# Kernel tuning notes

Hardware: AMD Instinct MI355X
Metric: run time of the kernel (lower is better)

## Reference

```python
import jax, jax.numpy as jnp
import numpy as np

EPS = 1e-5


def spline_conv(x, src, dst, pseudo, W, root, bias, num_nodes, K=5):
    """Degree-1 open B-spline conv (torch_spline_conv semantics), mean aggregation.
    W: [kernel_total, Cin, Cout]. kernel_total==1 means trivial basis (kernel_size=1)."""
    E = src.shape[0]
    Cin = x.shape[1]
    KT = W.shape[0]
    x_j = x[src]                                            # [E, Cin] edge gather
    deg = jax.ops.segment_sum(jnp.ones((E,), x.dtype), dst, num_segments=num_nodes)
    deg = jnp.maximum(deg, 1.0)
    if KT == 1:
        agg = jax.ops.segment_sum(x_j, dst, num_segments=num_nodes)
        out = (agg / deg[:, None]) @ W[0]
    else:
        v = pseudo * (K - 1)                                # open spline: v in [0, K-1]
        f = jnp.clip(jnp.floor(v), 0.0, K - 2)
        frac = v - f                                        # [E, 2]
        fi = f.astype(jnp.int32)
        # bucket basis-weighted source features by (kernel_index, dst) then one dense einsum
        h = jnp.zeros((KT * num_nodes, Cin), x.dtype)
        for s0 in (0, 1):
            for s1 in (0, 1):
                b0 = frac[:, 0] if s0 else 1.0 - frac[:, 0]
                b1 = frac[:, 1] if s1 else 1.0 - frac[:, 1]
                basis = b0 * b1                             # [E]
                wi = (fi[:, 0] + s0) + K * (fi[:, 1] + s1)  # [E] kernel index in [0,25)
                seg = wi * num_nodes + dst
                h = h + jax.ops.segment_sum(basis[:, None] * x_j, seg,
                                            num_segments=KT * num_nodes)
        agg = jnp.einsum('knc,kco->no', h.reshape(KT, num_nodes, Cin), W)
        out = agg / deg[:, None]
    return out + x @ root + bias


def batch_norm(x, gamma, beta):
    m = x.mean(axis=0)
    var = jnp.mean((x - m) ** 2, axis=0)
    return gamma * (x - m) * jax.lax.rsqrt(var + EPS) + beta


def setup_inputs() -> dict:
    key = jax.random.key(0)
    ks = jax.random.split(key, 8)
    N, E, Cin, Cout = 50000, 800000, 32, 64
    x = jax.random.normal(ks[0], (N, Cin), jnp.float32)
    edge_index = jax.random.randint(ks[1], (2, E), 0, N, jnp.int32)
    edge_attr = jax.random.uniform(ks[2], (E, 2), jnp.float32)
    s = 0.1
    return {
        'x': x, 'edge_index': edge_index, 'edge_attr': edge_attr,
        'w1': jax.random.normal(ks[3], (25, Cin, Cout), jnp.float32) * s,
        'r1': jax.random.normal(ks[4], (Cin, Cout), jnp.float32) * s,
        'b1': jnp.zeros((Cout,), jnp.float32),
        'g1': jnp.ones((Cout,), jnp.float32),
        'beta1': jnp.zeros((Cout,), jnp.float32),
        'w2': jax.random.normal(ks[5], (25, Cout, Cout), jnp.float32) * s,
        'r2': jax.random.normal(ks[6], (Cout, Cout), jnp.float32) * s,
        'b2': jnp.zeros((Cout,), jnp.float32),
        'g2': jnp.ones((Cout,), jnp.float32),
        'beta2': jnp.zeros((Cout,), jnp.float32),
        'ws': jax.random.normal(ks[7], (1, Cin, Cout), jnp.float32) * s,
        'rs': jax.random.normal(jax.random.fold_in(key, 99), (Cin, Cout), jnp.float32) * s,
        'bs': jnp.zeros((Cout,), jnp.float32),
        'gs': jnp.ones((Cout,), jnp.float32),
        'betas': jnp.zeros((Cout,), jnp.float32),
    }


def reference(x, edge_index, edge_attr, w1, r1, b1, g1, beta1,
              w2, r2, b2, g2, beta2, ws, rs, bs, gs, betas):
    N = x.shape[0]
    src, dst = edge_index[0], edge_index[1]
    h = jax.nn.elu(batch_norm(spline_conv(x, src, dst, edge_attr, w1, r1, b1, N), g1, beta1))
    left = batch_norm(spline_conv(h, src, dst, edge_attr, w2, r2, b2, N), g2, beta2)
    short = batch_norm(spline_conv(x, src, dst, edge_attr, ws, rs, bs, N), gs, betas)
    return jax.nn.elu(left + short)
```

## Files before the change

### kernel.cpp

```cpp
#include <hip/hip_runtime.h>

#define NN 50000
#define NE 800000
#define DBINS 1024

typedef __attribute__((ext_vector_type(8))) short bf16x8;
typedef __attribute__((ext_vector_type(4))) float f32x4;
typedef __attribute__((ext_vector_type(2))) float f32x2;

__device__ __forceinline__ unsigned short f2bf(float f) {
    union { float f; unsigned u; } v; v.f = f;
    unsigned r = v.u + 0x7FFFu + ((v.u >> 16) & 1u);
    return (unsigned short)(r >> 16);
}

__device__ __forceinline__ int4 ld_ep2(const int4* ep, unsigned idx, int which) {
    return *(const int4*)((const char*)ep + (size_t)(idx * 32u + (unsigned)which * 16u));
}
__device__ __forceinline__ unsigned ld_xu(const unsigned* X, unsigned byteoff) {
    return *(const unsigned*)((const char*)X + (size_t)byteoff);
}

__device__ __forceinline__ f32x2 unpack2(unsigned u) {
    union { unsigned u; float f; } a, b;
    a.u = u << 16;
    b.u = u & 0xFFFF0000u;
    return f32x2{a.f, b.f};
}

__device__ __forceinline__ f32x2 pk_mul_hib(f32x2 w, f32x2 x) {
    f32x2 d;
    asm("v_pk_mul_f32 %0, %1, %2 op_sel:[1,0] op_sel_hi:[1,1]"
        : "=v"(d) : "v"(w), "v"(x));
    return d;
}
__device__ __forceinline__ void pk_fma_lob(f32x2& h, f32x2 w, f32x2 t) {
    asm("v_pk_fma_f32 %0, %1, %2, %0 op_sel:[0,0,0] op_sel_hi:[0,1,1]"
        : "+v"(h) : "v"(w), "v"(t));
}

__device__ __forceinline__ int us_idx(int kk, int r, int m) {
    return kk*544 + (r >> 3)*136 + m*8 + (r & 7);
}
__device__ __forceinline__ int us8_idx(int kk, int r, int m) {
    return kk*272 + (r >> 3)*68 + m*8 + (r & 7);
}

template<bool HS>
__device__ __forceinline__ void edge_acc2(f32x2* h, f32x2& hs,
                                          const int4& pa, const int4& pb, f32x2 x) {
    f32x2 wxy[5];
    wxy[0] = unpack2((unsigned)pa.y);
    wxy[1] = unpack2((unsigned)pa.z);
    wxy[2] = unpack2((unsigned)pa.w);
    wxy[3] = unpack2((unsigned)pb.x);
    wxy[4] = unpack2((unsigned)pb.y);
    if (HS) hs += x;
#pragma unroll
    for (int r1 = 0; r1 < 5; ++r1) {
        f32x2 ty = pk_mul_hib(wxy[r1], x);
#pragma unroll
        for (int r0 = 0; r0 < 5; ++r0)
            pk_fma_lob(h[r1*5 + r0], wxy[r0], ty);
    }
}

__device__ __forceinline__ float eh_reduce(f32x2 v, int eh, int stride) {
    float mine  = eh ? v.y : v.x;
    float other = eh ? v.x : v.y;
    return mine + __shfl_xor(other, stride);
}

__global__ __launch_bounds__(256) void k_zero(int* degi, int* cur, float* stats,
                                              int* dcnt, int* dcur,
                                              unsigned* xz, unsigned* hz) {
    int i = blockIdx.x*256 + threadIdx.x;
    int stride = gridDim.x*256;
    for (int j = i; j < NN; j += stride) { degi[j] = 0; cur[j] = 0; }
    if (i < 384) stats[i] = 0.f;
    if (i < DBINS) { dcnt[i] = 0; dcur[i] = 0; }
    if (i < 16) xz[i] = 0u;
    if (i < 32) hz[i] = 0u;
}

__global__ __launch_bounds__(256) void k_hist(const int* __restrict__ dst, int* degi) {
    int e = blockIdx.x*256 + threadIdx.x;
    if (e < NE) atomicAdd(&degi[dst[e]], 1);
}

__global__ __launch_bounds__(256) void k_scan_block(const int* __restrict__ degi,
                                                    int* off, int* bsum) {
    __shared__ int sh[256];
    int t = threadIdx.x;
    int base = blockIdx.x * 1024;
    int v[4]; int s = 0;
#pragma unroll
    for (int j = 0; j < 4; j++) {
        int idx = base + t*4 + j;
        v[j] = (idx < NN) ? ((degi[idx] + 3) & ~3) : 0;
        s += v[j];
    }
    sh[t] = s; __syncthreads();
    for (int ofs = 1; ofs < 256; ofs <<= 1) {
        int x = (t >= ofs) ? sh[t - ofs] : 0;
        __syncthreads();
        sh[t] += x;
        __syncthreads();
    }
    int ex = sh[t] - s;
#pragma unroll
    for (int j = 0; j < 4; j++) {
        int idx = base + t*4 + j;
        if (idx < NN) off[idx] = ex;
        ex += v[j];
    }
    if (t == 255) bsum[blockIdx.x] = sh[255];
}

__global__ __launch_bounds__(256) void k_dhist(const int* __restrict__ degi, int* dcnt) {
    __shared__ int lh[DBINS];
    int t = threadIdx.x;
#pragma unroll
    for (int j = 0; j < DBINS/256; ++j) lh[t + 256*j] = 0;
    __syncthreads();
    int n = blockIdx.x*256 + t;
    if (n < NN) atomicAdd(&lh[min(degi[n], DBINS-1)], 1);
    __syncthreads();
#pragma unroll
    for (int j = 0; j < DBINS/256; ++j) {
        int b = t + 256*j;
        if (lh[b]) atomicAdd(&dcnt[b], lh[b]);
    }
}

__global__ __launch_bounds__(256) void k_topscan(const int* __restrict__ bsum,
                                                 int* bpre, int nb,
                                                 const int* __restrict__ dcnt,
                                                 int* dbase) {
    __shared__ int sh[256];
    int t = threadIdx.x;
    if (blockIdx.x == 0) {
        int s = (t < nb) ? bsum[t] : 0;
        sh[t] = s; __syncthreads();
        for (int ofs = 1; ofs < 256; ofs <<= 1) {
            int x = (t >= ofs) ? sh[t - ofs] : 0;
            __syncthreads();
            sh[t] += x;
            __syncthreads();
        }
        if (t < nb) bpre[t] = sh[t] - s;
    } else {
        int v[4]; int s = 0;
#pragma unroll
        for (int j = 0; j < 4; j++) { v[j] = dcnt[t*4 + j]; s += v[j]; }
        sh[t] = s; __syncthreads();
        for (int ofs = 1; ofs < 256; ofs <<= 1) {
            int x = (t >= ofs) ? sh[t - ofs] : 0;
            __syncthreads();
            sh[t] += x;
            __syncthreads();
        }
        int ex = sh[t] - s;
#pragma unroll
        for (int j = 0; j < 4; j++) { dbase[t*4 + j] = ex; ex += v[j]; }
    }
}

__global__ __launch_bounds__(256) void k_scan_add(int* off, const int* __restrict__ bpre,
                                                  const int* __restrict__ degi) {
    int i = blockIdx.x*256 + threadIdx.x;
    if (i < NN) {
        int v = off[i] + bpre[i >> 10];
        off[i] = v;
        if (i == NN - 1) off[NN] = v + ((degi[i] + 3) & ~3);
    }
}

__global__ __launch_bounds__(256) void k_pscatter_pad(const int* __restrict__ degi,
                                                      const int* __restrict__ dbase,
                                                      int* dcur, int* perm,
                                                      const int* __restrict__ off,
                                                      int4* __restrict__ ep) {
    __shared__ int lh[DBINS];
    __shared__ int lb[DBINS];
    int t = threadIdx.x;
#pragma unroll
    for (int j = 0; j < DBINS/256; ++j) lh[t + 256*j] = 0;
    __syncthreads();
    int n = blockIdx.x*256 + t;
    int d = 0, lr = 0;
    bool act = (n < NN);
    if (act) {
        d = min(degi[n], DBINS-1);
        lr = atomicAdd(&lh[d], 1);
    }
    __syncthreads();
#pragma unroll
    for (int j = 0; j < DBINS/256; ++j) {
        int b = t + 256*j;
        int c = lh[b];
        lb[b] = c ? atomicAdd(&dcur[b], c) : 0;
    }
    __syncthreads();
    if (act) {
        perm[dbase[d] + lb[d] + lr] = n;
        int base = off[n] + degi[n];
        int end  = off[n + 1];
        for (int p = base; p < end; ++p) {
            ep[2*p]     = make_int4(NN, 0, 0, 0);
            ep[2*p + 1] = make_int4(0, 0, 0, 0);
        }
    }
}

__global__ __launch_bounds__(256) void k_scatter(const int* __restrict__ src,
                                                 const int* __restrict__ dst,
                                                 const float* __restrict__ ea,
                                                 const int* __restrict__ off, int* cur,
                                                 int4* __restrict__ ep) {
    int e = blockIdx.x*256 + threadIdx.x;
    if (e >= NE) return;
    int d = dst[e];
    int p = off[d] + atomicAdd(&cur[d], 1);
    float v0 = ea[2*e]     * 4.f;
    float v1 = ea[2*e + 1] * 4.f;
    unsigned w[5];
#pragma unroll
    for (int r = 0; r < 5; ++r) {
        float wx = fmaxf(1.f - fabsf(v0 - (float)r), 0.f);
        float wy = fmaxf(1.f - fabsf(v1 - (float)r), 0.f);
        w[r] = (unsigned)f2bf(wx) | ((unsigned)f2bf(wy) << 16);
    }
    ep[2*p]     = make_int4(src[e], (int)w[0], (int)w[1], (int)w[2]);
    ep[2*p + 1] = make_int4((int)w[3], (int)w[4], 0, 0);
}

__device__ __forceinline__ void wprep_body(int tid, const float* W, const float* root,
                                           int KTC, unsigned short* Wb) {
    int lane = tid & 63, cot = (tid >> 6) & 3, kk = tid >> 8;
    int co = 16*cot + (lane & 15);
    int kbase = kk*32 + ((lane >> 4) * 8);
    union { unsigned short s[8]; uint4 v; } u;
#pragma unroll
    for (int j = 0; j < 8; j++) {
        int k = kbase + j;
        float val = (k < KTC) ? W[(size_t)k*64 + co] : root[(size_t)(k - KTC)*64 + co];
        u.s[j] = f2bf(val);
    }
    *(uint4*)(Wb + (size_t)tid * 8) = u.v;
}

__global__ __launch_bounds__(256) void k_prep(const float* __restrict__ x,
                                              unsigned short* __restrict__ xb,
                                              const float* __restrict__ w1,
                                              const float* __restrict__ r1,
                                              unsigned short* Wb1,
                                              const float* __restrict__ wsN,
                                              const float* __restrict__ rs,
                                              unsigned short* WbS,
                                              const float* __restrict__ w2,
                                              const float* __restrict__ r2,
                                              unsigned short* Wb2) {
    int b = blockIdx.x, t = threadIdx.x;
    if (b < 1563) {
        int i = b*256 + t;
        if (i >= NN*8) return;
        float4 v = ((const float4*)x)[i];
        uint2 pk;
        pk.x = (unsigned)f2bf(v.x) | ((unsigned)f2bf(v.y) << 16);
        pk.y = (unsigned)f2bf(v.z) | ((unsigned)f2bf(v.w) << 16);
        ((uint2*)xb)[i] = pk;
    } else if (b < 1589) {
        wprep_body((b - 1563)*256 + t, w1, r1, 800, Wb1);
    } else if (b < 1591) {
        wprep_body((b - 1589)*256 + t, wsN, rs, 32, WbS);
    } else {
        wprep_body((b - 1591)*256 + t, w2, r2, 1600, Wb2);
    }
}

__global__ __launch_bounds__(512, 4) void k_conv1s(
        const unsigned* __restrict__ Xbf,
        const int* __restrict__ off,
        const int* __restrict__ degi,
        const int4* __restrict__ ep,
        const int* __restrict__ perm,
        const unsigned short* __restrict__ Wb1,
        const unsigned short* __restrict__ WbS,
        const float* __restrict__ b1,
        const float* __restrict__ bs,
        float* __restrict__ agg1,
        float* __restrict__ aggS) {
    __shared__ __align__(16) unsigned short hb[28*544];
    const int t = threadIdx.x;
    const int g = t >> 5;
    const int q = t & 31;
    const int chp = q & 15;
    const int eh = q >> 4;
    const int n0 = blockIdx.x * 16;
    const int n = perm[n0 + g];

    f32x2 h[25], hs = {0.f, 0.f};
#pragma unroll
    for (int i = 0; i < 25; ++i) h[i] = f32x2{0.f, 0.f};

    const int ebeg = off[n], eend = off[n + 1];
    const float rdeg = 1.f / (float)max(degi[n], 1);

    for (int i = ebeg; i < eend; i += 4) {
        const unsigned i0 = (unsigned)(i + eh), i1 = (unsigned)(i + 2 + eh);
        int4 a0 = ld_ep2(ep, i0, 0), b0 = ld_ep2(ep, i0, 1);
        int4 a1 = ld_ep2(ep, i1, 0), b1 = ld_ep2(ep, i1, 1);
        unsigned u0 = ld_xu(Xbf, (unsigned)a0.x * 64u + (unsigned)chp * 4u);
        unsigned u1 = ld_xu(Xbf, (unsigned)a1.x * 64u + (unsigned)chp * 4u);
        edge_acc2<true>(h, hs, a0, b0, unpack2(u0));
        edge_acc2<true>(h, hs, a1, b1, unpack2(u1));
    }

    const int c = 2*chp + eh;
    const int bw = us_idx(0, c, g);
#pragma unroll
    for (int wi = 0; wi < 25; ++wi)
        hb[wi*544 + bw] = f2bf(eh_reduce(h[wi], eh, 16) * rdeg);
    hb[26*544 + bw] = f2bf(eh_reduce(hs, eh, 16) * rdeg);
    {
        unsigned ux = Xbf[(unsigned)n * 16u + (unsigned)chp];
        unsigned short xb = eh ? (unsigned short)(ux >> 16)
                               : (unsigned short)(ux & 0xFFFFu);
        hb[25*544 + bw] = xb;
        hb[27*544 + bw] = xb;
    }
    __syncthreads();

    const int lane = t & 63, w = t >> 6;
    const int m = lane & 15, qq = lane >> 4;
    const int co = (w & 3)*16 + m;
    const int4 pn = ((const int4*)perm)[(n0 >> 2) + qq];
    const int prow[4] = {pn.x, pn.y, pn.z, pn.w};
    if (w < 4) {
        f32x4 acc = {0.f, 0.f, 0.f, 0.f};
        for (int kk = 0; kk < 26; ++kk) {
            bf16x8 av = *(const bf16x8*)&hb[kk*544 + qq*136 + m*8];
            bf16x8 bv = *(const bf16x8*)(Wb1 + (size_t)((kk*4 + w)*64 + lane) * 8);
            acc = __builtin_amdgcn_mfma_f32_16x16x32_bf16(av, bv, acc, 0, 0, 0);
        }
        const float bb = b1[co];
#pragma unroll
        for (int r = 0; r < 4; ++r)
            agg1[(size_t)prow[r]*64 + co] = acc[r] + bb;
    } else {
        f32x4 accs = {0.f, 0.f, 0.f, 0.f};
#pragma unroll
        for (int s = 0; s < 2; ++s) {
            bf16x8 av = *(const bf16x8*)&hb[(26 + s)*544 + qq*136 + m*8];
            bf16x8 bv = *(const bf16x8*)(WbS + (size_t)((s*4 + (w & 3))*64 + lane) * 8);
            accs = __builtin_amdgcn_mfma_f32_16x16x32_bf16(av, bv, accs, 0, 0, 0);
        }
        const float bb = bs[co];
#pragma unroll
        for (int r = 0; r < 4; ++r)
            aggS[(size_t)prow[r]*64 + co] = accs[r] + bb;
    }
}

__global__ __launch_bounds__(256, 5) void k_conv2(
        const unsigned* __restrict__ Xbf,
        const int* __restrict__ off,
        const int* __restrict__ degi,
        const int4* __restrict__ ep,
        const int* __restrict__ perm,
        const unsigned short* __restrict__ Wb2,
        const float* __restrict__ b2,
        float* __restrict__ agg) {
    __shared__ __align__(16) unsigned short hb[52*272 + 256];
    const int t = threadIdx.x, lane = t & 63, w = t >> 6;
    const int n0 = blockIdx.x * 8;
    const int chp = lane & 31, eh = lane >> 5;
    const int c = 2*chp + eh;
    const int kh = c >> 5, r = c & 31;

#pragma unroll
    for (int nn = 0; nn < 2; ++nn) {
        const int g = 2*w + nn;
        const int n = perm[n0 + g];
        f32x2 h[25]; f32x2 hsd = {0.f, 0.f};
#pragma unroll
        for (int i = 0; i < 25; ++i) h[i] = f32x2{0.f, 0.f};

        const int ebeg = off[n], eend = off[n + 1];
        const float rdeg = 1.f / (float)max(degi[n], 1);

        for (int i = ebeg; i < eend; i += 4) {
            const unsigned i0 = (unsigned)(i + eh), i1 = (unsigned)(i + 2 + eh);
            int4 a0 = ld_ep2(ep, i0, 0), b0 = ld_ep2(ep, i0, 1);
            int4 a1 = ld_ep2(ep, i1, 0), b1 = ld_ep2(ep, i1, 1);
            unsigned u0 = ld_xu(Xbf, (unsigned)a0.x * 128u + (unsigned)chp * 4u);
            unsigned u1 = ld_xu(Xbf, (unsigned)a1.x * 128u + (unsigned)chp * 4u);
            edge_acc2<false>(h, hsd, a0, b0, unpack2(u0));
            edge_acc2<false>(h, hsd, a1, b1, unpack2(u1));
        }

        const int bw = us8_idx(0, r, g);
#pragma unroll
        for (int wi = 0; wi < 25; ++wi)
            hb[(wi*2 + kh)*272 + bw] = f2bf(eh_reduce(h[wi], eh, 32) * rdeg);
        {
            unsigned ux = Xbf[(unsigned)n * 32u + (unsigned)chp];
            hb[(50 + kh)*272 + bw] =
                (unsigned short)(eh ? (ux >> 16) : (ux & 0xFFFFu));
        }
    }
    __syncthreads();

    const int m = lane & 15, qq = lane >> 4;
    f32x4 acc = {0.f, 0.f, 0.f, 0.f};
    for (int kk = 0; kk < 52; ++kk) {
        bf16x8 av = *(const bf16x8*)&hb[kk*272 + qq*68 + m*8];
        bf16x8 bv = *(const bf16x8*)(Wb2 + (size_t)((kk*4 + w)*64 + lane) * 8);
        acc = __builtin_amdgcn_mfma_f32_16x16x32_bf16(av, bv, acc, 0, 0, 0);
    }
    if (qq < 2) {
        const int4 pn = ((const int4*)perm)[(n0 >> 2) + qq];
        const int prow[4] = {pn.x, pn.y, pn.z, pn.w};
        const int co = w*16 + m;
        const float bb = b2[co];
#pragma unroll
        for (int rr = 0; rr < 4; ++rr)
            agg[(size_t)prow[rr]*64 + co] = acc[rr] + bb;
    }
}

__global__ __launch_bounds__(256) void k_bnstats(const float* __restrict__ agg, float* stats) {
    __shared__ float sh0[256], sh1[256];
    int t = threadIdx.x;
    float s = 0.f, ss = 0.f;
    int stride = gridDim.x * 256;
    for (int i = blockIdx.x*256 + t; i < NN*64; i += stride) {
        float v = agg[i];
        s += v; ss += v*v;
    }
    sh0[t] = s; sh1[t] = ss;
    __syncthreads();
    if (t < 64) {
        float a = sh0[t] + sh0[t+64] + sh0[t+128] + sh0[t+192];
        float b = sh1[t] + sh1[t+64] + sh1[t+128] + sh1[t+192];
        atomicAdd(&stats[t], a);
        atomicAdd(&stats[64 + t], b);
    }
}

__global__ __launch_bounds__(256) void k_bnstats2(const float* __restrict__ a1,
                                                  const float* __restrict__ as,
                                                  float* stats) {
    __shared__ float sh0[256], sh1[256];
    int t = threadIdx.x;
    const float* src = (blockIdx.x < 256) ? a1 : as;
    float* dst = (blockIdx.x < 256) ? (stats + 128) : (stats + 256);
    int bid = (blockIdx.x < 256) ? blockIdx.x : blockIdx.x - 256;
    float s = 0.f, ss = 0.f;
    for (int i = bid*256 + t; i < NN*64; i += 256*256) {
        float v = src[i];
        s += v; ss += v*v;
    }
    sh0[t] = s; sh1[t] = ss;
    __syncthreads();
    if (t < 64) {
        float a = sh0[t] + sh0[t+64] + sh0[t+128] + sh0[t+192];
        float b = sh1[t] + sh1[t+64] + sh1[t+128] + sh1[t+192];
        atomicAdd(&dst[t], a);
        atomicAdd(&dst[64 + t], b);
    }
}

__device__ __forceinline__ float eluf(float u) { return u > 0.f ? u : expm1f(u); }

__global__ __launch_bounds__(256) void k_bn_elu(const float* __restrict__ agg,
                                                const float* __restrict__ stats,
                                                const float* __restrict__ gamma,
                                                const float* __restrict__ beta,
                                                unsigned short* __restrict__ outb) {
    int i = blockIdx.x*256 + threadIdx.x;
    if (i >= NN*16) return;
    float4 v = ((const float4*)agg)[i];
    float r[4] = {v.x, v.y, v.z, v.w};
    int c0 = (i << 2) & 63;
#pragma unroll
    for (int j = 0; j < 4; j++) {
        int c = c0 + j;
        float mu = stats[c] * (1.f/NN);
        float var = stats[64 + c] * (1.f/NN) - mu*mu;
        float sc = gamma[c] * rsqrtf(fmaxf(var, 0.f) + 1e-5f);
        r[j] = eluf((r[j] - mu)*sc + beta[c]);
    }
    uint2 pk;
    pk.x = (unsigned)f2bf(r[0]) | ((unsigned)f2bf(r[1]) << 16);
    pk.y = (unsigned)f2bf(r[2]) | ((unsigned)f2bf(r[3]) << 16);
    ((uint2*)outb)[i] = pk;
}

__global__ __launch_bounds__(256) void k_bn_final(const float* __restrict__ a2,
                                                  const float* __restrict__ st2,
                                                  const float* __restrict__ g2,
                                                  const float* __restrict__ be2,
                                                  const float* __restrict__ as,
                                                  const float* __restrict__ sts,
                                                  const float* __restrict__ gs,
                                                  const float* __restrict__ bes,
                                                  float* __restrict__ out) {
    int i = blockIdx.x*256 + threadIdx.x;
    if (i >= NN*16) return;
    float4 v2 = ((const float4*)a2)[i];
    float4 vs = ((const float4*)as)[i];
    float r2v[4] = {v2.x, v2.y, v2.z, v2.w};
    float rsv[4] = {vs.x, vs.y, vs.z, vs.w};
    float o[4];
    int c0 = (i << 2) & 63;
#pragma unroll
    for (int j = 0; j < 4; j++) {
        int c = c0 + j;
        float mu2 = st2[c] * (1.f/NN);
        float var2 = st2[64 + c] * (1.f/NN) - mu2*mu2;
        float sc2 = g2[c] * rsqrtf(fmaxf(var2, 0.f) + 1e-5f);
        float mus = sts[c] * (1.f/NN);
        float vars = sts[64 + c] * (1.f/NN) - mus*mus;
        float scs = gs[c] * rsqrtf(fmaxf(vars, 0.f) + 1e-5f);
        float u = (r2v[j] - mu2)*sc2 + be2[c] + (rsv[j] - mus)*scs + bes[c];
        o[j] = eluf(u);
    }
    ((float4*)out)[i] = make_float4(o[0], o[1], o[2], o[3]);
}

extern "C" void kernel_launch(void* const* d_in, const int* in_sizes, int n_in,
                              void* d_out, int out_size, void* d_ws, size_t ws_size,
                              hipStream_t stream) {
    const float* x   = (const float*)d_in[0];
    const int*   ei  = (const int*)d_in[1];
    const float* ea  = (const float*)d_in[2];
    const float* w1  = (const float*)d_in[3];
    const float* r1  = (const float*)d_in[4];
    const float* b1  = (const float*)d_in[5];
    const float* g1  = (const float*)d_in[6];
    const float* be1 = (const float*)d_in[7];
    const float* w2  = (const float*)d_in[8];
    const float* r2  = (const float*)d_in[9];
    const float* b2  = (const float*)d_in[10];
    const float* g2  = (const float*)d_in[11];
    const float* be2 = (const float*)d_in[12];
    const float* wsN = (const float*)d_in[13];
    const float* rs  = (const float*)d_in[14];
    const float* bs  = (const float*)d_in[15];
    const float* gs  = (const float*)d_in[16];
    const float* bes = (const float*)d_in[17];
    const int* srcp = ei;
    const int* dstp = ei + NE;

    char* wsb = (char*)d_ws;
    size_t o = 0;
    auto alloc = [&](size_t bytes) -> char* {
        char* p = wsb + o;
        o += (bytes + 255) & ~(size_t)255;
        return p;
    };
    int*    degi    = (int*)   alloc((size_t)NN * 4);
    int*    cur     = (int*)   alloc((size_t)NN * 4);
    int*    off     = (int*)   alloc((size_t)(NN + 1) * 4);
    int*    bsum    = (int*)   alloc(256 * 4);
    int*    bpre    = (int*)   alloc(256 * 4);
    int*    dcnt    = (int*)   alloc(DBINS * 4);
    int*    dcur    = (int*)   alloc(DBINS * 4);
    int*    dbase   = (int*)   alloc(DBINS * 4);
    int*    perm    = (int*)   alloc((size_t)NN * 4);
    int4*   ep      = (int4*)  alloc(((size_t)NE + 3*NN + 64) * 32);
    unsigned short* Wb1 = (unsigned short*)alloc(26 * 4096);
    unsigned short* WbS = (unsigned short*)alloc(2 * 4096);
    unsigned short* Wb2 = (unsigned short*)alloc(52 * 4096);
    float*  agg1    = (float*) alloc((size_t)NN * 64 * 4);
    float*  aggS    = (float*) alloc((size_t)NN * 64 * 4);
    unsigned short* h1bf = (unsigned short*)alloc((size_t)(NN + 1) * 64 * 2);
    unsigned short* xbf  = (unsigned short*)alloc((size_t)(NN + 1) * 32 * 2);
    float*  stats   = (float*) alloc(384 * 4);
    (void)ws_size; (void)in_sizes; (void)n_in; (void)out_size;

    float* out = (float*)d_out;

    k_zero<<<196, 256, 0, stream>>>(degi, cur, stats, dcnt, dcur,
                                    (unsigned*)(xbf + (size_t)NN * 32),
                                    (unsigned*)(h1bf + (size_t)NN * 64));
    k_hist<<<3125, 256, 0, stream>>>(dstp, degi);
    k_scan_block<<<49, 256, 0, stream>>>(degi, off, bsum);
    k_dhist<<<196, 256, 0, stream>>>(degi, dcnt);
    k_topscan<<<2, 256, 0, stream>>>(bsum, bpre, 49, dcnt, dbase);
    k_scan_add<<<196, 256, 0, stream>>>(off, bpre, degi);
    k_pscatter_pad<<<196, 256, 0, stream>>>(degi, dbase, dcur, perm, off, ep);
    k_scatter<<<3125, 256, 0, stream>>>(srcp, dstp, ea, off, cur, ep);

    k_prep<<<1643, 256, 0, stream>>>(x, xbf, w1, r1, Wb1, wsN, rs, WbS, w2, r2, Wb2);

    k_conv1s<<<3125, 512, 0, stream>>>((const unsigned*)xbf, off, degi, ep, perm,
                                       Wb1, WbS, b1, bs, agg1, aggS);
    k_bnstats<<<256, 256, 0, stream>>>(agg1, stats);
    k_bn_elu<<<3125, 256, 0, stream>>>(agg1, stats, g1, be1, h1bf);

    k_conv2<<<6250, 256, 0, stream>>>((const unsigned*)h1bf, off, degi, ep, perm,
                                      Wb2, b2, agg1);
    k_bnstats2<<<512, 256, 0, stream>>>(agg1, aggS, stats);
    k_bn_final<<<3125, 256, 0, stream>>>(agg1, stats + 128, g2, be2,
                                         aggS, stats + 256, gs, bes, out);
}
```

Measured before the change: 427.6 us.

## Restructure conv2 to one 32-lane group per node, 16 nodes per block

k_conv2 now runs 512-thread blocks covering 16 nodes, with each 32-thread half-wave processing one node's edges sequentially over all 64 channels. Before, each wave handled 2 nodes with edges split across half-waves and a cross-lane reduction. This removes the eh_reduce shuffle and gives the MFMA tiles a full 16 rows instead of 8 useful ones. The staged hidden buffer is written in two halves with extra barriers so shared memory stays small, but only 4 of the 8 waves issue MFMAs, and per-node serial edge loops may worsen imbalance across degrees.

```diff
diff --git a/kernel.cpp b/kernel.cpp
--- a/kernel.cpp
+++ b/kernel.cpp
@@ -41,9 +41,6 @@
 
 __device__ __forceinline__ int us_idx(int kk, int r, int m) {
     return kk*544 + (r >> 3)*136 + m*8 + (r & 7);
-}
-__device__ __forceinline__ int us8_idx(int kk, int r, int m) {
-    return kk*272 + (r >> 3)*68 + m*8 + (r & 7);
 }
 
 template<bool HS>
@@ -363,7 +360,7 @@
     }
 }
 
-__global__ __launch_bounds__(256, 5) void k_conv2(
+__global__ __launch_bounds__(512, 6) void k_conv2(
         const unsigned* __restrict__ Xbf,
         const int* __restrict__ off,
         const int* __restrict__ degi,
@@ -372,62 +369,75 @@
         const unsigned short* __restrict__ Wb2,
         const float* __restrict__ b2,
         float* __restrict__ agg) {
-    __shared__ __align__(16) unsigned short hb[52*272 + 256];
+    __shared__ __align__(16) unsigned short hb[26*544];
+    unsigned* hb32 = (unsigned*)hb;
     const int t = threadIdx.x, lane = t & 63, w = t >> 6;
-    const int n0 = blockIdx.x * 8;
-    const int chp = lane & 31, eh = lane >> 5;
-    const int c = 2*chp + eh;
-    const int kh = c >> 5, r = c & 31;
-
-#pragma unroll
-    for (int nn = 0; nn < 2; ++nn) {
-        const int g = 2*w + nn;
-        const int n = perm[n0 + g];
-        f32x2 h[25]; f32x2 hsd = {0.f, 0.f};
-#pragma unroll
-        for (int i = 0; i < 25; ++i) h[i] = f32x2{0.f, 0.f};
-
-        const int ebeg = off[n], eend = off[n + 1];
-        const float rdeg = 1.f / (float)max(degi[n], 1);
-
-        for (int i = ebeg; i < eend; i += 4) {
-            const unsigned i0 = (unsigned)(i + eh), i1 = (unsigned)(i + 2 + eh);
-            int4 a0 = ld_ep2(ep, i0, 0), b0 = ld_ep2(ep, i0, 1);
-            int4 a1 = ld_ep2(ep, i1, 0), b1 = ld_ep2(ep, i1, 1);
-            unsigned u0 = ld_xu(Xbf, (unsigned)a0.x * 128u + (unsigned)chp * 4u);
-            unsigned u1 = ld_xu(Xbf, (unsigned)a1.x * 128u + (unsigned)chp * 4u);
-            edge_acc2<false>(h, hsd, a0, b0, unpack2(u0));
-            edge_acc2<false>(h, hsd, a1, b1, unpack2(u1));
-        }
-
-        const int bw = us8_idx(0, r, g);
-#pragma unroll
-        for (int wi = 0; wi < 25; ++wi)
-            hb[(wi*2 + kh)*272 + bw] = f2bf(eh_reduce(h[wi], eh, 32) * rdeg);
-        {
-            unsigned ux = Xbf[(unsigned)n * 32u + (unsigned)chp];
-            hb[(50 + kh)*272 + bw] =
-                (unsigned short)(eh ? (ux >> 16) : (ux & 0xFFFFu));
-        }
+    const int n0 = blockIdx.x * 16;
+    const int g = t >> 5;
+    const int chp = t & 31;
+    const int n = perm[n0 + g];
+
+    f32x2 h[25];
+#pragma unroll
+    for (int i = 0; i < 25; ++i) h[i] = f32x2{0.f, 0.f};
+
+    const int ebeg = off[n], eend = off[n + 1];
+    const float rdeg = 1.f / (float)max(degi[n], 1);
+
+    for (int i = ebeg; i < eend; i += 2) {
+        int4 a0 = ld_ep2(ep, (unsigned)i, 0),       b0 = ld_ep2(ep, (unsigned)i, 1);
+        int4 a1 = ld_ep2(ep, (unsigned)(i+1), 0),   b1 = ld_ep2(ep, (unsigned)(i+1), 1);
+        unsigned u0 = ld_xu(Xbf, (unsigned)a0.x * 128u + (unsigned)chp * 4u);
+        unsigned u1 = ld_xu(Xbf, (unsigned)a1.x * 128u + (unsigned)chp * 4u);
+        f32x2 dummy = {0.f, 0.f};
+        edge_acc2<false>(h, dummy, a0, b0, unpack2(u0));
+        edge_acc2<false>(h, dummy, a1, b1, unpack2(u1));
+    }
+
+    const int kh = chp >> 4;
+    const int r0 = (2*chp) & 31;
+    const int dw = us_idx(0, r0, g) >> 1;
+#pragma unroll
+    for (int wi = 0; wi <= 12; ++wi) {
+        unsigned pk = (unsigned)f2bf(h[wi].x * rdeg)
+                    | ((unsigned)f2bf(h[wi].y * rdeg) << 16);
+        hb32[(unsigned)(2*wi + kh)*272u + dw] = pk;
     }
     __syncthreads();
 
     const int m = lane & 15, qq = lane >> 4;
     f32x4 acc = {0.f, 0.f, 0.f, 0.f};
-    for (int kk = 0; kk < 52; ++kk) {
-        bf16x8 av = *(const bf16x8*)&hb[kk*272 + qq*68 + m*8];
-        bf16x8 bv = *(const bf16x8*)(Wb2 + (size_t)((kk*4 + w)*64 + lane) * 8);
+    if (w < 4) {
+        for (int kk = 0; kk < 26; ++kk) {
+            bf16x8 av = *(const bf16x8*)&hb[kk*544 + qq*136 + m*8];
+            bf16x8 bv = *(const bf16x8*)(Wb2 + (size_t)((kk*4 + w)*64 + lane) * 8);
+            acc = __builtin_amdgcn_mfma_f32_16x16x32_bf16(av, bv, acc, 0, 0, 0);
+        }
+    }
+    __syncthreads();
+
+#pragma unroll
+    for (int wi = 13; wi < 25; ++wi) {
+        unsigned pk = (unsigned)f2bf(h[wi].x * rdeg)
+                    | ((unsigned)f2bf(h[wi].y * rdeg) << 16);
+        hb32[(unsigned)(2*wi + kh - 26)*272u + dw] = pk;
+    }
+    hb32[(unsigned)(24 + kh)*272u + dw] = Xbf[(unsigned)n * 32u + (unsigned)chp];
+    __syncthreads();
+
+    if (w >= 4) return;
+    for (int kk = 0; kk < 26; ++kk) {
+        bf16x8 av = *(const bf16x8*)&hb[kk*544 + qq*136 + m*8];
+        bf16x8 bv = *(const bf16x8*)(Wb2 + (size_t)(((kk + 26)*4 + w)*64 + lane) * 8);
         acc = __builtin_amdgcn_mfma_f32_16x16x32_bf16(av, bv, acc, 0, 0, 0);
     }
-    if (qq < 2) {
-        const int4 pn = ((const int4*)perm)[(n0 >> 2) + qq];
-        const int prow[4] = {pn.x, pn.y, pn.z, pn.w};
-        const int co = w*16 + m;
-        const float bb = b2[co];
-#pragma unroll
-        for (int rr = 0; rr < 4; ++rr)
-            agg[(size_t)prow[rr]*64 + co] = acc[rr] + bb;
-    }
+    const int4 pn = ((const int4*)perm)[(n0 >> 2) + qq];
+    const int prow[4] = {pn.x, pn.y, pn.z, pn.w};
+    const int co = w*16 + m;
+    const float bb = b2[co];
+#pragma unroll
+    for (int rr = 0; rr < 4; ++rr)
+        agg[(size_t)prow[rr]*64 + co] = acc[rr] + bb;
 }
 
 __global__ __launch_bounds__(256) void k_bnstats(const float* __restrict__ agg, float* stats) {
@@ -601,7 +611,7 @@
     k_bnstats<<<256, 256, 0, stream>>>(agg1, stats);
     k_bn_elu<<<3125, 256, 0, stream>>>(agg1, stats, g1, be1, h1bf);
 
-    k_conv2<<<6250, 256, 0, stream>>>((const unsigned*)h1bf, off, degi, ep, perm,
+    k_conv2<<<3125, 512, 0, stream>>>((const unsigned*)h1bf, off, degi, ep, perm,
                                       Wb2, b2, agg1);
     k_bnstats2<<<512, 256, 0, stream>>>(agg1, aggS, stats);
     k_bn_final<<<3125, 256, 0, stream>>>(agg1, stats + 128, g2, be2,
```

Result: no change. 427.2 us (-0.1%).

## Compute per-node spline aggregation with MFMA over precomputed 2D basis weights

Applied to the files above, without the earlier changes.

The scatter kernel now precomputes the full 25-entry bilinear basis product per edge, plus a constant-one slot for the shortcut sum, and stores it in a separate bf16 array alongside a plain source-index array. The per-node edge aggregation in both conv kernels then becomes an MFMA matmul (basis weights times gathered source features) in place of scalar packed FMAs. conv2 also moves to 512-thread blocks of 16 nodes, node order is reversed to start from the high-degree end, and conv1 occupancy bounds are raised. The cost is larger per-edge storage (64 bytes of weights instead of 32), gathers of scattered 2-byte elements, and idle MFMA lanes for low-degree nodes.

```diff
diff --git a/kernel.cpp b/kernel.cpp
--- a/kernel.cpp
+++ b/kernel.cpp
@@ -6,7 +6,6 @@
 
 typedef __attribute__((ext_vector_type(8))) short bf16x8;
 typedef __attribute__((ext_vector_type(4))) float f32x4;
-typedef __attribute__((ext_vector_type(2))) float f32x2;
 
 __device__ __forceinline__ unsigned short f2bf(float f) {
     union { float f; unsigned u; } v; v.f = f;
@@ -14,61 +13,54 @@
     return (unsigned short)(r >> 16);
 }
 
-__device__ __forceinline__ int4 ld_ep2(const int4* ep, unsigned idx, int which) {
-    return *(const int4*)((const char*)ep + (size_t)(idx * 32u + (unsigned)which * 16u));
-}
-__device__ __forceinline__ unsigned ld_xu(const unsigned* X, unsigned byteoff) {
-    return *(const unsigned*)((const char*)X + (size_t)byteoff);
-}
-
-__device__ __forceinline__ f32x2 unpack2(unsigned u) {
-    union { unsigned u; float f; } a, b;
-    a.u = u << 16;
-    b.u = u & 0xFFFF0000u;
-    return f32x2{a.f, b.f};
-}
-
-__device__ __forceinline__ f32x2 pk_mul_hib(f32x2 w, f32x2 x) {
-    f32x2 d;
-    asm("v_pk_mul_f32 %0, %1, %2 op_sel:[1,0] op_sel_hi:[1,1]"
-        : "=v"(d) : "v"(w), "v"(x));
-    return d;
-}
-__device__ __forceinline__ void pk_fma_lob(f32x2& h, f32x2 w, f32x2 t) {
-    asm("v_pk_fma_f32 %0, %1, %2, %0 op_sel:[0,0,0] op_sel_hi:[0,1,1]"
-        : "+v"(h) : "v"(w), "v"(t));
-}
-
 __device__ __forceinline__ int us_idx(int kk, int r, int m) {
     return kk*544 + (r >> 3)*136 + m*8 + (r & 7);
 }
-__device__ __forceinline__ int us8_idx(int kk, int r, int m) {
-    return kk*272 + (r >> 3)*68 + m*8 + (r & 7);
-}
-
-template<bool HS>
-__device__ __forceinline__ void edge_acc2(f32x2* h, f32x2& hs,
-                                          const int4& pa, const int4& pb, f32x2 x) {
-    f32x2 wxy[5];
-    wxy[0] = unpack2((unsigned)pa.y);
-    wxy[1] = unpack2((unsigned)pa.z);
-    wxy[2] = unpack2((unsigned)pa.w);
-    wxy[3] = unpack2((unsigned)pb.x);
-    wxy[4] = unpack2((unsigned)pb.y);
-    if (HS) hs += x;
-#pragma unroll
-    for (int r1 = 0; r1 < 5; ++r1) {
-        f32x2 ty = pk_mul_hib(wxy[r1], x);
-#pragma unroll
-        for (int r0 = 0; r0 < 5; ++r0)
-            pk_fma_lob(h[r1*5 + r0], wxy[r0], ty);
-    }
-}
-
-__device__ __forceinline__ float eh_reduce(f32x2 v, int eh, int stride) {
-    float mine  = eh ? v.y : v.x;
-    float other = eh ? v.x : v.y;
-    return mine + __shfl_xor(other, stride);
+
+template<int CIN, int NT>
+__device__ __forceinline__ void stage1_node(
+        const int* __restrict__ epsrc,
+        const unsigned short* __restrict__ wfull,
+        const unsigned short* __restrict__ Xh,
+        int ebeg, int degp, int lane,
+        f32x4 (&d)[2][NT]) {
+#pragma unroll
+    for (int mt = 0; mt < 2; ++mt)
+#pragma unroll
+        for (int nt = 0; nt < NT; ++nt)
+            d[mt][nt] = f32x4{0.f, 0.f, 0.f, 0.f};
+    if (degp <= 0) return;
+    const int l15 = lane & 15;
+    const int kb = (lane >> 4) * 8;
+    const int last = degp - 1;
+    for (int k0 = 0; k0 < degp; k0 += 32) {
+        int e[8]; int s[8]; bool val[8];
+#pragma unroll
+        for (int j = 0; j < 8; ++j) {
+            int k = k0 + kb + j;
+            val[j] = (k < degp);
+            e[j] = ebeg + min(k, last);
+        }
+#pragma unroll
+        for (int j = 0; j < 8; ++j) s[j] = epsrc[e[j]];
+        union { unsigned short us[8]; bf16x8 v; } a0, a1;
+#pragma unroll
+        for (int j = 0; j < 8; ++j) {
+            unsigned short w0 = wfull[(size_t)e[j]*32 + l15];
+            unsigned short w1 = wfull[(size_t)e[j]*32 + 16 + l15];
+            a0.us[j] = val[j] ? w0 : (unsigned short)0;
+            a1.us[j] = val[j] ? w1 : (unsigned short)0;
+        }
+#pragma unroll
+        for (int nt = 0; nt < NT; ++nt) {
+            union { unsigned short us[8]; bf16x8 v; } b;
+#pragma unroll
+            for (int j = 0; j < 8; ++j)
+                b.us[j] = Xh[(size_t)s[j]*CIN + nt*16 + l15];
+            d[0][nt] = __builtin_amdgcn_mfma_f32_16x16x32_bf16(a0.v, b.v, d[0][nt], 0, 0, 0);
+            d[1][nt] = __builtin_amdgcn_mfma_f32_16x16x32_bf16(a1.v, b.v, d[1][nt], 0, 0, 0);
+        }
+    }
 }
 
 __global__ __launch_bounds__(256) void k_zero(int* degi, int* cur, float* stats,
@@ -180,7 +172,8 @@
                                                       const int* __restrict__ dbase,
                                                       int* dcur, int* perm,
                                                       const int* __restrict__ off,
-                                                      int4* __restrict__ ep) {
+                                                      int* __restrict__ epsrc,
+                                                      unsigned short* __restrict__ wfull) {
     __shared__ int lh[DBINS];
     __shared__ int lb[DBINS];
     int t = threadIdx.x;
@@ -206,9 +199,11 @@
         perm[dbase[d] + lb[d] + lr] = n;
         int base = off[n] + degi[n];
         int end  = off[n + 1];
+        uint4 z = make_uint4(0u, 0u, 0u, 0u);
         for (int p = base; p < end; ++p) {
-            ep[2*p]     = make_int4(NN, 0, 0, 0);
-            ep[2*p + 1] = make_int4(0, 0, 0, 0);
+            epsrc[p] = NN;
+            uint4* wp = (uint4*)(wfull + (size_t)p * 32);
+            wp[0] = z; wp[1] = z; wp[2] = z; wp[3] = z;
         }
     }
 }
@@ -217,22 +212,32 @@
                                                  const int* __restrict__ dst,
                                                  const float* __restrict__ ea,
                                                  const int* __restrict__ off, int* cur,
-                                                 int4* __restrict__ ep) {
+                                                 int* __restrict__ epsrc,
+                                                 unsigned short* __restrict__ wfull) {
     int e = blockIdx.x*256 + threadIdx.x;
     if (e >= NE) return;
     int d = dst[e];
     int p = off[d] + atomicAdd(&cur[d], 1);
     float v0 = ea[2*e]     * 4.f;
     float v1 = ea[2*e + 1] * 4.f;
-    unsigned w[5];
+    float wx[5], wy[5];
 #pragma unroll
     for (int r = 0; r < 5; ++r) {
-        float wx = fmaxf(1.f - fabsf(v0 - (float)r), 0.f);
-        float wy = fmaxf(1.f - fabsf(v1 - (float)r), 0.f);
-        w[r] = (unsigned)f2bf(wx) | ((unsigned)f2bf(wy) << 16);
-    }
-    ep[2*p]     = make_int4(src[e], (int)w[0], (int)w[1], (int)w[2]);
-    ep[2*p + 1] = make_int4((int)w[3], (int)w[4], 0, 0);
+        wx[r] = fmaxf(1.f - fabsf(v0 - (float)r), 0.f);
+        wy[r] = fmaxf(1.f - fabsf(v1 - (float)r), 0.f);
+    }
+    union { unsigned short s[32]; uint4 q[4]; } u;
+#pragma unroll
+    for (int r1 = 0; r1 < 5; ++r1)
+#pragma unroll
+        for (int r0 = 0; r0 < 5; ++r0)
+            u.s[r1*5 + r0] = f2bf(wx[r0] * wy[r1]);
+    u.s[25] = 0x3F80;
+#pragma unroll
+    for (int i = 26; i < 32; ++i) u.s[i] = 0;
+    epsrc[p] = src[e];
+    uint4* wp = (uint4*)(wfull + (size_t)p * 32);
+    wp[0] = u.q[0]; wp[1] = u.q[1]; wp[2] = u.q[2]; wp[3] = u.q[3];
 }
 
 __device__ __forceinline__ void wprep_body(int tid, const float* W, const float* root,
@@ -279,11 +284,12 @@
     }
 }
 
-__global__ __launch_bounds__(512, 4) void k_conv1s(
-        const unsigned* __restrict__ Xbf,
+__global__ __launch_bounds__(512, 6) void k_conv1s(
+        const unsigned short* __restrict__ Xh,
         const int* __restrict__ off,
         const int* __restrict__ degi,
-        const int4* __restrict__ ep,
+        const int* __restrict__ epsrc,
+        const unsigned short* __restrict__ wfull,
         const int* __restrict__ perm,
         const unsigned short* __restrict__ Wb1,
         const unsigned short* __restrict__ WbS,
@@ -292,48 +298,48 @@
         float* __restrict__ agg1,
         float* __restrict__ aggS) {
     __shared__ __align__(16) unsigned short hb[28*544];
-    const int t = threadIdx.x;
-    const int g = t >> 5;
-    const int q = t & 31;
-    const int chp = q & 15;
-    const int eh = q >> 4;
-    const int n0 = blockIdx.x * 16;
-    const int n = perm[n0 + g];
-
-    f32x2 h[25], hs = {0.f, 0.f};
-#pragma unroll
-    for (int i = 0; i < 25; ++i) h[i] = f32x2{0.f, 0.f};
-
-    const int ebeg = off[n], eend = off[n + 1];
-    const float rdeg = 1.f / (float)max(degi[n], 1);
-
-    for (int i = ebeg; i < eend; i += 4) {
-        const unsigned i0 = (unsigned)(i + eh), i1 = (unsigned)(i + 2 + eh);
-        int4 a0 = ld_ep2(ep, i0, 0), b0 = ld_ep2(ep, i0, 1);
-        int4 a1 = ld_ep2(ep, i1, 0), b1 = ld_ep2(ep, i1, 1);
-        unsigned u0 = ld_xu(Xbf, (unsigned)a0.x * 64u + (unsigned)chp * 4u);
-        unsigned u1 = ld_xu(Xbf, (unsigned)a1.x * 64u + (unsigned)chp * 4u);
-        edge_acc2<true>(h, hs, a0, b0, unpack2(u0));
-        edge_acc2<true>(h, hs, a1, b1, unpack2(u1));
-    }
-
-    const int c = 2*chp + eh;
-    const int bw = us_idx(0, c, g);
-#pragma unroll
-    for (int wi = 0; wi < 25; ++wi)
-        hb[wi*544 + bw] = f2bf(eh_reduce(h[wi], eh, 16) * rdeg);
-    hb[26*544 + bw] = f2bf(eh_reduce(hs, eh, 16) * rdeg);
-    {
-        unsigned ux = Xbf[(unsigned)n * 16u + (unsigned)chp];
-        unsigned short xb = eh ? (unsigned short)(ux >> 16)
-                               : (unsigned short)(ux & 0xFFFFu);
-        hb[25*544 + bw] = xb;
-        hb[27*544 + bw] = xb;
-    }
-    __syncthreads();
-
-    const int lane = t & 63, w = t >> 6;
-    const int m = lane & 15, qq = lane >> 4;
+    unsigned* hb32 = (unsigned*)hb;
+    const int t = threadIdx.x, lane = t & 63, w = t >> 6;
+    const int n0 = NN - 16 - blockIdx.x * 16;
+    const int l15 = lane & 15;
+    const int wib = (lane >> 4) * 4;
+
+#pragma unroll
+    for (int nn = 0; nn < 2; ++nn) {
+        const int g = 2*w + nn;
+        const int n = perm[n0 + g];
+        const int deg = degi[n];
+        const int degp = (deg + 3) & ~3;
+        f32x4 d[2][2];
+        stage1_node<32, 2>(epsrc, wfull, Xh, off[n], degp, lane, d);
+        const float rdeg = 1.f / (float)max(deg, 1);
+        const int basel = (l15 >> 3)*136 + g*8 + (l15 & 7);
+#pragma unroll
+        for (int mt = 0; mt < 2; ++mt)
+#pragma unroll
+            for (int nt = 0; nt < 2; ++nt)
+#pragma unroll
+                for (int r = 0; r < 4; ++r) {
+                    int wi = mt*16 + wib + r;
+                    if (wi <= 25) {
+                        int kk = (wi < 25) ? wi : 26;
+                        hb[kk*544 + nt*272 + basel] = f2bf(d[mt][nt][r] * rdeg);
+                    }
+                }
+    }
+    if ((lane & 31) < 16) {
+        const int g2 = 2*w + (lane >> 5);
+        const int cd = lane & 15;
+        const int n2 = perm[n0 + g2];
+        unsigned xv = ((const unsigned*)Xh)[(size_t)n2*16 + cd];
+        const int r0 = 2*cd;
+        const int dwb = (r0 >> 3)*68 + g2*4 + ((r0 & 7) >> 1);
+        hb32[25*272 + dwb] = xv;
+        hb32[27*272 + dwb] = xv;
+    }
+    __syncthreads();
+
+    const int m = l15, qq = lane >> 4;
     const int co = (w & 3)*16 + m;
     const int4 pn = ((const int4*)perm)[(n0 >> 2) + qq];
     const int prow[4] = {pn.x, pn.y, pn.z, pn.w};
@@ -363,71 +369,72 @@
     }
 }
 
-__global__ __launch_bounds__(256, 5) void k_conv2(
-        const unsigned* __restrict__ Xbf,
+__global__ __launch_bounds__(512, 4) void k_conv2(
+        const unsigned short* __restrict__ Xh,
         const int* __restrict__ off,
         const int* __restrict__ degi,
-        const int4* __restrict__ ep,
+        const int* __restrict__ epsrc,
+        const unsigned short* __restrict__ wfull,
         const int* __restrict__ perm,
         const unsigned short* __restrict__ Wb2,
         const float* __restrict__ b2,
         float* __restrict__ agg) {
-    __shared__ __align__(16) unsigned short hb[52*272 + 256];
+    __shared__ __align__(16) unsigned short hb[52*544];
+    unsigned* hb32 = (unsigned*)hb;
     const int t = threadIdx.x, lane = t & 63, w = t >> 6;
-    const int n0 = blockIdx.x * 8;
-    const int chp = lane & 31, eh = lane >> 5;
-    const int c = 2*chp + eh;
-    const int kh = c >> 5, r = c & 31;
+    const int n0 = NN - 16 - blockIdx.x * 16;
+    const int l15 = lane & 15;
+    const int wib = (lane >> 4) * 4;
 
 #pragma unroll
     for (int nn = 0; nn < 2; ++nn) {
         const int g = 2*w + nn;
         const int n = perm[n0 + g];
-        f32x2 h[25]; f32x2 hsd = {0.f, 0.f};
-#pragma unroll
-        for (int i = 0; i < 25; ++i) h[i] = f32x2{0.f, 0.f};
-
-        const int ebeg = off[n], eend = off[n + 1];
-        const float rdeg = 1.f / (float)max(degi[n], 1);
-
-        for (int i = ebeg; i < eend; i += 4) {
-            const unsigned i0 = (unsigned)(i + eh), i1 = (unsigned)(i + 2 + eh);
-            int4 a0 = ld_ep2(ep, i0, 0), b0 = ld_ep2(ep, i0, 1);
-            int4 a1 = ld_ep2(ep, i1, 0), b1 = ld_ep2(ep, i1, 1);
-            unsigned u0 = ld_xu(Xbf, (unsigned)a0.x * 128u + (unsigned)chp * 4u);
-            unsigned u1 = ld_xu(Xbf, (unsigned)a1.x * 128u + (unsigned)chp * 4u);
-            edge_acc2<false>(h, hsd, a0, b0, unpack2(u0));
-            edge_acc2<false>(h, hsd, a1, b1, unpack2(u1));
-        }
-
-        const int bw = us8_idx(0, r, g);
-#pragma unroll
-        for (int wi = 0; wi < 25; ++wi)
-            hb[(wi*2 + kh)*272 + bw] = f2bf(eh_reduce(h[wi], eh, 32) * rdeg);
-        {
-            unsigned ux = Xbf[(unsigned)n * 32u + (unsigned)chp];
-            hb[(50 + kh)*272 + bw] =
-                (unsigned short)(eh ? (ux >> 16) : (ux & 0xFFFFu));
-        }
-    }
-    __syncthreads();
-
-    const int m = lane & 15, qq = lane >> 4;
+        const int deg = degi[n];
+        const int degp = (deg + 3) & ~3;
+        f32x4 d[2][4];
+        stage1_node<64, 4>(epsrc, wfull, Xh, off[n], degp, lane, d);
+        const float rdeg = 1.f / (float)max(deg, 1);
+        const int basel = (l15 >> 3)*136 + g*8 + (l15 & 7);
+#pragma unroll
+        for (int mt = 0; mt < 2; ++mt)
+#pragma unroll
+            for (int nt = 0; nt < 4; ++nt) {
+                const int cadd = (nt >> 1)*544 + (nt & 1)*272 + basel;
+#pragma unroll
+                for (int r = 0; r < 4; ++r) {
+                    int wi = mt*16 + wib + r;
+                    if (wi < 25)
+                        hb[wi*1088 + cadd] = f2bf(d[mt][nt][r] * rdeg);
+                }
+            }
+    }
+    {
+        const int g2 = 2*w + (lane >> 5);
+        const int c2 = lane & 31;
+        const int n2 = perm[n0 + g2];
+        unsigned xv = ((const unsigned*)Xh)[(size_t)n2*32 + c2];
+        const int r0 = (2*c2) & 31;
+        const int dw = (50 + (c2 >> 4))*272 + (r0 >> 3)*68 + g2*4 + ((r0 & 7) >> 1);
+        hb32[dw] = xv;
+    }
+    __syncthreads();
+
+    if (w >= 4) return;
+    const int m = l15, qq = lane >> 4;
     f32x4 acc = {0.f, 0.f, 0.f, 0.f};
     for (int kk = 0; kk < 52; ++kk) {
-        bf16x8 av = *(const bf16x8*)&hb[kk*272 + qq*68 + m*8];
+        bf16x8 av = *(const bf16x8*)&hb[kk*544 + qq*136 + m*8];
         bf16x8 bv = *(const bf16x8*)(Wb2 + (size_t)((kk*4 + w)*64 + lane) * 8);
         acc = __builtin_amdgcn_mfma_f32_16x16x32_bf16(av, bv, acc, 0, 0, 0);
     }
-    if (qq < 2) {
-        const int4 pn = ((const int4*)perm)[(n0 >> 2) + qq];
-        const int prow[4] = {pn.x, pn.y, pn.z, pn.w};
-        const int co = w*16 + m;
-        const float bb = b2[co];
-#pragma unroll
-        for (int rr = 0; rr < 4; ++rr)
-            agg[(size_t)prow[rr]*64 + co] = acc[rr] + bb;
-    }
+    const int4 pn = ((const int4*)perm)[(n0 >> 2) + qq];
+    const int prow[4] = {pn.x, pn.y, pn.z, pn.w};
+    const int co = w*16 + m;
+    const float bb = b2[co];
+#pragma unroll
+    for (int rr = 0; rr < 4; ++rr)
+        agg[(size_t)prow[rr]*64 + co] = acc[rr] + bb;
 }
 
 __global__ __launch_bounds__(256) void k_bnstats(const float* __restrict__ agg, float* stats) {
@@ -570,7 +577,8 @@
     int*    dcur    = (int*)   alloc(DBINS * 4);
     int*    dbase   = (int*)   alloc(DBINS * 4);
     int*    perm    = (int*)   alloc((size_t)NN * 4);
-    int4*   ep      = (int4*)  alloc(((size_t)NE + 3*NN + 64) * 32);
+    int*    epsrc   = (int*)   alloc(((size_t)NE + 3*NN + 64) * 4);
+    unsigned short* wfull = (unsigned short*)alloc(((size_t)NE + 3*NN + 64) * 64);
     unsigned short* Wb1 = (unsigned short*)alloc(26 * 4096);
     unsigned short* WbS = (unsigned short*)alloc(2 * 4096);
     unsigned short* Wb2 = (unsigned short*)alloc(52 * 4096);
@@ -591,17 +599,17 @@
     k_dhist<<<196, 256, 0, stream>>>(degi, dcnt);
     k_topscan<<<2, 256, 0, stream>>>(bsum, bpre, 49, dcnt, dbase);
     k_scan_add<<<196, 256, 0, stream>>>(off, bpre, degi);
-    k_pscatter_pad<<<196, 256, 0, stream>>>(degi, dbase, dcur, perm, off, ep);
-    k_scatter<<<3125, 256, 0, stream>>>(srcp, dstp, ea, off, cur, ep);
+    k_pscatter_pad<<<196, 256, 0, stream>>>(degi, dbase, dcur, perm, off, epsrc, wfull);
+    k_scatter<<<3125, 256, 0, stream>>>(srcp, dstp, ea, off, cur, epsrc, wfull);
 
     k_prep<<<1643, 256, 0, stream>>>(x, xbf, w1, r1, Wb1, wsN, rs, WbS, w2, r2, Wb2);
 
-    k_conv1s<<<3125, 512, 0, stream>>>((const unsigned*)xbf, off, degi, ep, perm,
+    k_conv1s<<<3125, 512, 0, stream>>>(xbf, off, degi, epsrc, wfull, perm,
                                        Wb1, WbS, b1, bs, agg1, aggS);
     k_bnstats<<<256, 256, 0, stream>>>(agg1, stats);
     k_bn_elu<<<3125, 256, 0, stream>>>(agg1, stats, g1, be1, h1bf);
 
-    k_conv2<<<6250, 256, 0, stream>>>((const unsigned*)h1bf, off, degi, ep, perm,
+    k_conv2<<<3125, 512, 0, stream>>>(h1bf, off, degi, epsrc, wfull, perm,
                                       Wb2, b2, agg1);
     k_bnstats2<<<512, 256, 0, stream>>>(agg1, aggS, stats);
     k_bn_final<<<3125, 256, 0, stream>>>(agg1, stats + 128, g2, be2,
```

After: 431.5 us. About the same (+0.9%).
